# Performance work log

Hardware: AMD Instinct MI355X
Metric: run time of the kernel (lower is better)

The kernel has to match this reference:

```python
import jax, jax.numpy as jnp
import numpy as np

D_MODEL = 1024
N_LAYERS = 4
N_HEADS = 16
HEAD_DIM = 64
FF_DIM = 4096
INNER = N_HEADS * HEAD_DIM  # 1024
SCALE = HEAD_DIM ** -0.5
EPS = 1e-5


def layernorm(x, scale, bias):
    mu = jnp.mean(x, axis=-1, keepdims=True)
    var = jnp.mean(jnp.square(x - mu), axis=-1, keepdims=True)
    return (x - mu) * jax.lax.rsqrt(var + EPS) * scale + bias


def setup_inputs() -> dict:
    key = jax.random.key(0)
    ks = jax.random.split(key, 8)
    b, n = 2, 2048
    s = lambda fan_in: 1.0 / np.sqrt(fan_in)
    inp = {
        "x": jax.random.normal(ks[0], (b, n, D_MODEL), dtype=jnp.float32),
        "Wqkv": jax.random.normal(ks[1], (N_LAYERS, D_MODEL, 3 * INNER), dtype=jnp.float32) * s(D_MODEL),
        "Wout": jax.random.normal(ks[2], (N_LAYERS, INNER, D_MODEL), dtype=jnp.float32) * s(INNER),
        "ln1_s": jnp.ones((N_LAYERS, D_MODEL), jnp.float32),
        "ln1_b": jnp.zeros((N_LAYERS, D_MODEL), jnp.float32),
        "W1": jax.random.normal(ks[3], (N_LAYERS, D_MODEL, FF_DIM), dtype=jnp.float32) * s(D_MODEL),
        "b1": jnp.zeros((N_LAYERS, FF_DIM), jnp.float32),
        "W2": jax.random.normal(ks[4], (N_LAYERS, FF_DIM, D_MODEL), dtype=jnp.float32) * s(FF_DIM),
        "b2": jnp.zeros((N_LAYERS, D_MODEL), jnp.float32),
        "ln2_s": jnp.ones((N_LAYERS, D_MODEL), jnp.float32),
        "ln2_b": jnp.zeros((N_LAYERS, D_MODEL), jnp.float32),
        "lnf_s": jnp.ones((D_MODEL,), jnp.float32),
        "lnf_b": jnp.zeros((D_MODEL,), jnp.float32),
    }
    return inp


def reference(x, Wqkv, Wout, ln1_s, ln1_b, W1, b1, W2, b2, ln2_s, ln2_b, lnf_s, lnf_b):
    b, n, _ = x.shape
    for i in range(N_LAYERS):
        # --- attention block (pre-norm, residual) ---
        h = layernorm(x, ln1_s[i], ln1_b[i])
        qkv = h @ Wqkv[i]                                  # [b, n, 3*inner]
        q, k, v = jnp.split(qkv, 3, axis=-1)
        def heads(t):
            return t.reshape(b, n, N_HEADS, HEAD_DIM).transpose(0, 2, 1, 3)  # b h n d
        q, k, v = heads(q), heads(k), heads(v)
        dots = jnp.einsum('bhnd,bhmd->bhnm', q, k) * SCALE
        attn = jax.nn.softmax(dots, axis=-1)
        out = jnp.einsum('bhnm,bhmd->bhnd', attn, v)
        out = out.transpose(0, 2, 1, 3).reshape(b, n, INNER)
        x = out @ Wout[i] + x
        # --- feedforward block (pre-norm, residual) ---
        h = layernorm(x, ln2_s[i], ln2_b[i])
        h = jax.nn.gelu(h @ W1[i] + b1[i], approximate=False)  # torch GELU default = exact erf
        x = h @ W2[i] + b2[i] + x
    return layernorm(x, lnf_s, lnf_b)
```

## Files before the change

### kernel.cpp

```cpp
#include <hip/hip_runtime.h>
#include <math.h>

#define D_MODEL 1024
#define N_LAYERS 4
#define N_HEADS 16
#define HEAD_DIM 64
#define FF_DIM 4096
#define INNER 1024
#define QKV3 3072
#define EPS 1e-5f
#define ATT_SCALE 0.125f

typedef unsigned short u16;
typedef __attribute__((ext_vector_type(8))) short bf16x8;
typedef __attribute__((ext_vector_type(4))) float f32x4;

typedef const void __attribute__((address_space(1)))* gas1_t;
typedef void __attribute__((address_space(3)))* las3_t;

__device__ __forceinline__ void gl_lds16(const void* g, void* l) {
    __builtin_amdgcn_global_load_lds((gas1_t)g, (las3_t)l, 16, 0, 0);
}
__device__ __forceinline__ void lds_fence() {
    asm volatile("s_waitcnt lgkmcnt(0)" ::: "memory");
    __builtin_amdgcn_sched_barrier(0);
}

__device__ __forceinline__ u16 bf_of(float x) {
    unsigned u = __float_as_uint(x);
    unsigned r = (u + 0x7fffu + ((u >> 16) & 1u)) >> 16;
    return (u16)r;
}
__device__ __forceinline__ float f_of_bf(u16 b) {
    return __uint_as_float(((unsigned)b) << 16);
}
__device__ __forceinline__ void split2(float x, u16& h, u16& l) {
    h = bf_of(x);
    l = bf_of(x - f_of_bf(h));
}

template<bool SPLIT>
__global__ __launch_bounds__(256) void ln_kernel(const float* __restrict__ in,
                                                 const float* __restrict__ sc,
                                                 const float* __restrict__ bs,
                                                 float* outf, u16* outh, u16* outl)
{
    int row = blockIdx.x;
    int t = threadIdx.x;
    const float4* x4 = (const float4*)(in + (size_t)row * D_MODEL);
    float4 v = x4[t];
    float sum = v.x + v.y + v.z + v.w;
    float sq  = v.x*v.x + v.y*v.y + v.z*v.z + v.w*v.w;
#pragma unroll
    for (int o = 32; o > 0; o >>= 1) {
        sum += __shfl_xor(sum, o);
        sq  += __shfl_xor(sq, o);
    }
    __shared__ float s1[4], s2[4];
    int w = t >> 6;
    if ((t & 63) == 0) { s1[w] = sum; s2[w] = sq; }
    __syncthreads();
    sum = s1[0] + s1[1] + s1[2] + s1[3];
    sq  = s2[0] + s2[1] + s2[2] + s2[3];
    float mu  = sum * (1.0f / D_MODEL);
    float var = sq * (1.0f / D_MODEL) - mu * mu;
    float rs  = rsqrtf(var + EPS);
    float4 s = ((const float4*)sc)[t];
    float4 b = ((const float4*)bs)[t];
    float o0 = (v.x - mu) * rs * s.x + b.x;
    float o1 = (v.y - mu) * rs * s.y + b.y;
    float o2 = (v.z - mu) * rs * s.z + b.z;
    float o3 = (v.w - mu) * rs * s.w + b.w;
    if (SPLIT) {
        u16 h0,l0,h1,l1,h2,l2,h3,l3;
        split2(o0,h0,l0); split2(o1,h1,l1); split2(o2,h2,l2); split2(o3,h3,l3);
        size_t idx = (size_t)row * D_MODEL + t * 4;
        *(ushort4*)&outh[idx] = make_ushort4(h0,h1,h2,h3);
        *(ushort4*)&outl[idx] = make_ushort4(l0,l1,l2,l3);
    } else {
        ((float4*)(outf + (size_t)row * D_MODEL))[t] = make_float4(o0,o1,o2,o3);
    }
}

__global__ __launch_bounds__(256) void wsplit_kernel(const float* __restrict__ W,
                                                     u16* __restrict__ Th,
                                                     u16* __restrict__ Tl,
                                                     int K, int N)
{
    __shared__ float t[32][33];
    int tx = threadIdx.x & 31, ty = threadIdx.x >> 5;
    int n0 = blockIdx.x * 32, k0 = blockIdx.y * 32;
#pragma unroll
    for (int i = 0; i < 4; i++) {
        int r = ty + i * 8;
        t[r][tx] = W[(size_t)(k0 + r) * N + n0 + tx];
    }
    __syncthreads();
#pragma unroll
    for (int i = 0; i < 4; i++) {
        int r = ty + i * 8;
        float v = t[tx][r];
        u16 h, l; split2(v, h, l);
        size_t idx = (size_t)(n0 + r) * K + k0 + tx;
        Th[idx] = h; Tl[idx] = l;
    }
}

__global__ __launch_bounds__(256) void vtprep(const u16* __restrict__ qh,
                                              const u16* __restrict__ ql,
                                              u16* __restrict__ vth,
                                              u16* __restrict__ vtl, int n)
{
    int bh = blockIdx.y;
    int b = bh >> 4, h = bh & 15;
    int nb = blockIdx.x * 64 + (threadIdx.x >> 6) * 16;
    int d = threadIdx.x & 63;
    const u16* srcH = qh + (size_t)(b * n + nb) * QKV3 + 2 * INNER + h * HEAD_DIM + d;
    const u16* srcL = ql + (size_t)(b * n + nb) * QKV3 + 2 * INNER + h * HEAD_DIM + d;
    u16 bh_[16], bl_[16];
#pragma unroll
    for (int i = 0; i < 16; i++) {
        bh_[i] = srcH[(size_t)i * QKV3];
        bl_[i] = srcL[(size_t)i * QKV3];
    }
    size_t drow = ((size_t)bh * HEAD_DIM + d) * n + nb;
    *(uint4*)&vth[drow]     = *(uint4*)&bh_[0];
    *(uint4*)&vth[drow + 8] = *(uint4*)&bh_[8];
    *(uint4*)&vtl[drow]     = *(uint4*)&bl_[0];
    *(uint4*)&vtl[drow + 8] = *(uint4*)&bl_[8];
}

#define MFMA_BF16 __builtin_amdgcn_mfma_f32_16x16x32_bf16

template<bool BIAS, bool RES, bool GELU_, bool SPLITOUT>
__global__ __launch_bounds__(256, 2) void mfma_gemm(
    const u16* __restrict__ Ah, const u16* __restrict__ Al,
    const u16* __restrict__ Bh, const u16* __restrict__ Bl,
    const float* __restrict__ bias, const float* res,
    float* Cf, u16* Ch, u16* Cl,
    int M, int N, int K)
{
    __shared__ u16 Asm[128 * 64];
    __shared__ u16 Bsm[128 * 64];
    const int tid = threadIdx.x;
    const int bm0 = blockIdx.y * 128, bn0 = blockIdx.x * 128;
    const int wave = tid >> 6, lane = tid & 63;
    const int wm0 = (wave >> 1) * 64, wn0 = (wave & 1) * 64;
    const int fr = lane & 15, fp = lane >> 4;

    const u16* srcA[4]; const u16* srcB[4];
    u16* dstA[4]; u16* dstB[4];
#pragma unroll
    for (int s = 0; s < 4; s++) {
        int t_ = wave * 4 + s;
        int c  = t_ * 64 + lane;
        int r  = c >> 3;
        int q  = (c & 7) ^ (r & 7);
        const u16* Asel = (q & 4) ? Al : Ah;
        const u16* Bsel = (q & 4) ? Bl : Bh;
        srcA[s] = Asel + (size_t)(bm0 + r) * K + (q & 3) * 8;
        srcB[s] = Bsel + (size_t)(bn0 + r) * K + (q & 3) * 8;
        dstA[s] = &Asm[t_ * 512];
        dstB[s] = &Bsm[t_ * 512];
    }

    const bf16x8 *pAh[4], *pAl[4], *pBh[4], *pBl[4];
#pragma unroll
    for (int i = 0; i < 4; i++) {
        int Ra = wm0 + i * 16 + fr, Rb = wn0 + i * 16 + fr;
        int s7 = fr & 7;
        pAh[i] = (const bf16x8*)&Asm[(Ra * 8 + (fp ^ s7)) * 8];
        pAl[i] = (const bf16x8*)&Asm[(Ra * 8 + ((fp + 4) ^ s7)) * 8];
        pBh[i] = (const bf16x8*)&Bsm[(Rb * 8 + (fp ^ s7)) * 8];
        pBl[i] = (const bf16x8*)&Bsm[(Rb * 8 + ((fp + 4) ^ s7)) * 8];
    }

    f32x4 acc[4][4];
#pragma unroll
    for (int i = 0; i < 4; i++)
#pragma unroll
        for (int j = 0; j < 4; j++)
#pragma unroll
            for (int q = 0; q < 4; q++) acc[i][j][q] = 0.0f;

    for (int k0 = 0; k0 < K; k0 += 32) {
        __syncthreads();
#pragma unroll
        for (int s = 0; s < 4; s++) {
            gl_lds16(srcA[s] + k0, dstA[s]);
            gl_lds16(srcB[s] + k0, dstB[s]);
        }
        __syncthreads();

        bf16x8 fah[4], fal[4], fbh[4], fbl[4];
#pragma unroll
        for (int i = 0; i < 4; i++) {
            fah[i] = *pAh[i]; fal[i] = *pAl[i];
            fbh[i] = *pBh[i]; fbl[i] = *pBl[i];
        }
#pragma unroll
        for (int i = 0; i < 4; i++)
#pragma unroll
            for (int j = 0; j < 4; j++) {
                acc[i][j] = MFMA_BF16(fah[i], fbh[j], acc[i][j], 0, 0, 0);
                acc[i][j] = MFMA_BF16(fah[i], fbl[j], acc[i][j], 0, 0, 0);
                acc[i][j] = MFMA_BF16(fal[i], fbh[j], acc[i][j], 0, 0, 0);
            }
    }

#pragma unroll
    for (int i = 0; i < 4; i++)
#pragma unroll
        for (int j = 0; j < 4; j++) {
            int col = bn0 + wn0 + j * 16 + fr;
            float bv = BIAS ? bias[col] : 0.0f;
#pragma unroll
            for (int q = 0; q < 4; q++) {
                int row = bm0 + wm0 + i * 16 + fp * 4 + q;
                float t = acc[i][j][q] + bv;
                if (GELU_) t = 0.5f * t * (1.0f + erff(t * 0.70710678118654752f));
                if (RES) t += res[(size_t)row * N + col];
                size_t idx = (size_t)row * N + col;
                if (SPLITOUT) { u16 h, l; split2(t, h, l); Ch[idx] = h; Cl[idx] = l; }
                else Cf[idx] = t;
            }
        }
}

__global__ __launch_bounds__(256, 2) void attn_mfma(
    const u16* __restrict__ qh, const u16* __restrict__ ql,
    const u16* __restrict__ vth, const u16* __restrict__ vtl,
    u16* __restrict__ oh, u16* __restrict__ ol, int n, int qblocks)
{
    __shared__ u16 Kt[2][64 * 64];
    __shared__ u16 Vt[2][64 * 64];
    __shared__ u16 Pb[4][2][16 * 64];

    int total = gridDim.x;
    int per_xcd = total >> 3;
    int g = blockIdx.x;
    int flat = (g & 7) * per_xcd + (g >> 3);
    int bh = flat / qblocks;
    int qb = flat - bh * qblocks;
    int b = bh >> 4, h = bh & 15;
    int q0 = qb * 64;

    const int tid = threadIdx.x;
    const int wave = tid >> 6, lane = tid & 63;
    const int q_ = lane & 15, qx = q_ & 7;

    bf16x8 qfh[2], qfl[2];
    {
        size_t qo = (size_t)(b * n + q0 + wave * 16 + q_) * QKV3
                  + h * HEAD_DIM + (lane >> 4) * 8;
        qfh[0] = *(const bf16x8*)&qh[qo];
        qfh[1] = *(const bf16x8*)&qh[qo + 32];
        qfl[0] = *(const bf16x8*)&ql[qo];
        qfl[1] = *(const bf16x8*)&ql[qo + 32];
    }

    f32x4 oa[4];
#pragma unroll
    for (int dt = 0; dt < 4; dt++)
#pragma unroll
        for (int r = 0; r < 4; r++) oa[dt][r] = 0.0f;
    float mreg = -1e30f, lreg = 0.0f;

    for (int j0 = 0; j0 < n; j0 += 64) {
        __syncthreads();
#pragma unroll
        for (int e = 0; e < 8; e++) {
            int ei = wave * 8 + e;
            int half = (ei >> 3) & 1;
            int cb = ei & 7;
            int c = cb * 64 + lane;
            int r = c >> 3;
            int p = (c & 7) ^ (r & 7);
            if (ei < 16) {
                const u16* src = (half ? ql : qh)
                    + (size_t)(b * n + j0 + r) * QKV3 + INNER + h * HEAD_DIM + p * 8;
                gl_lds16(src, &Kt[half][cb * 512]);
            } else {
                const u16* src = (half ? vtl : vth)
                    + ((size_t)bh * HEAD_DIM + r) * n + j0 + p * 8;
                gl_lds16(src, &Vt[half][cb * 512]);
            }
        }
        __syncthreads();

        f32x4 sa[4];
#pragma unroll
        for (int jt = 0; jt < 4; jt++) {
#pragma unroll
            for (int r = 0; r < 4; r++) sa[jt][r] = 0.0f;
            int jr = jt * 16 + q_;
            int ro = jr * 64, x7 = jr & 7;
#pragma unroll
            for (int ks = 0; ks < 2; ks++) {
                int sl = (ks * 4 + (lane >> 4)) ^ x7;
                bf16x8 kh_ = *(const bf16x8*)&Kt[0][ro + sl * 8];
                bf16x8 kl_ = *(const bf16x8*)&Kt[1][ro + sl * 8];
                sa[jt] = MFMA_BF16(kh_, qfh[ks], sa[jt], 0, 0, 0);
                sa[jt] = MFMA_BF16(kh_, qfl[ks], sa[jt], 0, 0, 0);
                sa[jt] = MFMA_BF16(kl_, qfh[ks], sa[jt], 0, 0, 0);
            }
        }

        float p[16];
        float mt = -1e30f;
#pragma unroll
        for (int jt = 0; jt < 4; jt++)
#pragma unroll
            for (int r = 0; r < 4; r++) {
                float sv = sa[jt][r] * ATT_SCALE;
                p[jt * 4 + r] = sv;
                mt = fmaxf(mt, sv);
            }
        mt = fmaxf(mt, __shfl_xor(mt, 16));
        mt = fmaxf(mt, __shfl_xor(mt, 32));
        float mn = fmaxf(mreg, mt);
        float al = __expf(mreg - mn);
        float ps = 0.0f;
#pragma unroll
        for (int t = 0; t < 16; t++) { p[t] = __expf(p[t] - mn); ps += p[t]; }
        ps += __shfl_xor(ps, 16);
        ps += __shfl_xor(ps, 32);
        lreg = lreg * al + ps;
        mreg = mn;
#pragma unroll
        for (int dt = 0; dt < 4; dt++)
#pragma unroll
            for (int r = 0; r < 4; r++) oa[dt][r] *= al;

#pragma unroll
        for (int jt = 0; jt < 4; jt++) {
            int jb = jt * 16 + (lane >> 4) * 4;
            int uo = q_ * 64 + (((jb >> 3) ^ qx) * 8) + (jb & 7);
            ushort4 wh, wl;
            split2(p[jt * 4 + 0], wh.x, wl.x);
            split2(p[jt * 4 + 1], wh.y, wl.y);
            split2(p[jt * 4 + 2], wh.z, wl.z);
            split2(p[jt * 4 + 3], wh.w, wl.w);
            *(ushort4*)&Pb[wave][0][uo] = wh;
            *(ushort4*)&Pb[wave][1][uo] = wl;
        }
        lds_fence();

#pragma unroll
        for (int dt = 0; dt < 4; dt++) {
            int dr = dt * 16 + q_;
            int rv = dr * 64, d7 = dr & 7;
#pragma unroll
            for (int js = 0; js < 2; js++) {
                int sl = js * 4 + (lane >> 4);
                bf16x8 vh_ = *(const bf16x8*)&Vt[0][rv + ((sl ^ d7) * 8)];
                bf16x8 vl_ = *(const bf16x8*)&Vt[1][rv + ((sl ^ d7) * 8)];
                int po = q_ * 64 + ((sl ^ qx) * 8);
                bf16x8 ph_ = *(const bf16x8*)&Pb[wave][0][po];
                bf16x8 pl_ = *(const bf16x8*)&Pb[wave][1][po];
                oa[dt] = MFMA_BF16(vh_, ph_, oa[dt], 0, 0, 0);
                oa[dt] = MFMA_BF16(vh_, pl_, oa[dt], 0, 0, 0);
                oa[dt] = MFMA_BF16(vl_, ph_, oa[dt], 0, 0, 0);
            }
        }
    }

    float inv = 1.0f / lreg;
#pragma unroll
    for (int dt = 0; dt < 4; dt++) {
        int db = dt * 16 + (lane >> 4) * 4;
        int uo = q_ * 64 + (((db >> 3) ^ qx) * 8) + (db & 7);
        ushort4 wh, wl;
        split2(oa[dt][0] * inv, wh.x, wl.x);
        split2(oa[dt][1] * inv, wh.y, wl.y);
        split2(oa[dt][2] * inv, wh.z, wl.z);
        split2(oa[dt][3] * inv, wh.w, wl.w);
        *(ushort4*)&Pb[wave][0][uo] = wh;
        *(ushort4*)&Pb[wave][1][uo] = wl;
    }
    lds_fence();
#pragma unroll
    for (int pass = 0; pass < 2; pass++) {
        int qq = lane >> 2;
        int sl = (lane & 3) + pass * 4;
        int uo = qq * 64 + ((sl ^ (qq & 7)) * 8);
        bf16x8 vh_ = *(const bf16x8*)&Pb[wave][0][uo];
        bf16x8 vl_ = *(const bf16x8*)&Pb[wave][1][uo];
        size_t orow = (size_t)(b * n + q0 + wave * 16 + qq) * INNER
                    + h * HEAD_DIM + sl * 8;
        *(bf16x8*)&oh[orow] = vh_;
        *(bf16x8*)&ol[orow] = vl_;
    }
}

extern "C" void kernel_launch(void* const* d_in, const int* in_sizes, int n_in,
                              void* d_out, int out_size, void* d_ws, size_t ws_size,
                              hipStream_t stream)
{
    const float* x_in   = (const float*)d_in[0];
    const float* Wqkv   = (const float*)d_in[1];
    const float* Wout   = (const float*)d_in[2];
    const float* ln1_s  = (const float*)d_in[3];
    const float* ln1_b  = (const float*)d_in[4];
    const float* W1     = (const float*)d_in[5];
    const float* b1     = (const float*)d_in[6];
    const float* W2     = (const float*)d_in[7];
    const float* b2     = (const float*)d_in[8];
    const float* ln2_s  = (const float*)d_in[9];
    const float* ln2_b  = (const float*)d_in[10];
    const float* lnf_s  = (const float*)d_in[11];
    const float* lnf_b  = (const float*)d_in[12];
    float* outp = (float*)d_out;

    int rows = in_sizes[0] / D_MODEL;
    int n = 2048;
    int batch = rows / n;
    int nbh = batch * N_HEADS;
    int qblocks = n / 64;

    char* p = (char*)d_ws;
    float* x = (float*)p;  p += (size_t)rows * D_MODEL * 4;
    u16* hh  = (u16*)p;    p += (size_t)rows * D_MODEL * 2;
    u16* hl  = (u16*)p;    p += (size_t)rows * D_MODEL * 2;
    u16* qkvh = (u16*)p;
    u16* ffh  = (u16*)p;   p += (size_t)rows * FF_DIM * 2;
    u16* qkvl = (u16*)p;
    u16* ffl  = (u16*)p;   p += (size_t)rows * FF_DIM * 2;
    u16* vth = (u16*)p;    p += (size_t)nbh * HEAD_DIM * n * 2;
    u16* vtl = (u16*)p;    p += (size_t)nbh * HEAD_DIM * n * 2;
    u16* wbh = (u16*)p;    p += (size_t)FF_DIM * D_MODEL * 2;
    u16* wbl = (u16*)p;    p += (size_t)FF_DIM * D_MODEL * 2;

    hipMemcpyAsync(x, x_in, (size_t)rows * D_MODEL * 4, hipMemcpyDeviceToDevice, stream);

    dim3 blk(256);
    for (int i = 0; i < N_LAYERS; i++) {
        const float* Wqkv_i = Wqkv + (size_t)i * D_MODEL * QKV3;
        const float* Wout_i = Wout + (size_t)i * INNER * D_MODEL;
        const float* W1_i   = W1 + (size_t)i * D_MODEL * FF_DIM;
        const float* W2_i   = W2 + (size_t)i * FF_DIM * D_MODEL;

        wsplit_kernel<<<dim3(QKV3/32, D_MODEL/32), blk, 0, stream>>>(Wqkv_i, wbh, wbl, D_MODEL, QKV3);
        ln_kernel<true><<<rows, blk, 0, stream>>>(x, ln1_s + i*D_MODEL, ln1_b + i*D_MODEL,
                                                  nullptr, hh, hl);
        mfma_gemm<false,false,false,true><<<dim3(QKV3/128, rows/128), blk, 0, stream>>>(
            hh, hl, wbh, wbl, nullptr, nullptr, nullptr, qkvh, qkvl, rows, QKV3, D_MODEL);
        vtprep<<<dim3(n/64, nbh), blk, 0, stream>>>(qkvh, qkvl, vth, vtl, n);
        attn_mfma<<<nbh * qblocks, blk, 0, stream>>>(qkvh, qkvl, vth, vtl, hh, hl, n, qblocks);
        wsplit_kernel<<<dim3(D_MODEL/32, INNER/32), blk, 0, stream>>>(Wout_i, wbh, wbl, INNER, D_MODEL);
        mfma_gemm<false,true,false,false><<<dim3(D_MODEL/128, rows/128), blk, 0, stream>>>(
            hh, hl, wbh, wbl, nullptr, x, x, nullptr, nullptr, rows, D_MODEL, INNER);

        ln_kernel<true><<<rows, blk, 0, stream>>>(x, ln2_s + i*D_MODEL, ln2_b + i*D_MODEL,
                                                  nullptr, hh, hl);
        wsplit_kernel<<<dim3(FF_DIM/32, D_MODEL/32), blk, 0, stream>>>(W1_i, wbh, wbl, D_MODEL, FF_DIM);
        mfma_gemm<true,false,true,true><<<dim3(FF_DIM/128, rows/128), blk, 0, stream>>>(
            hh, hl, wbh, wbl, b1 + (size_t)i*FF_DIM, nullptr, nullptr, ffh, ffl,
            rows, FF_DIM, D_MODEL);
        wsplit_kernel<<<dim3(D_MODEL/32, FF_DIM/32), blk, 0, stream>>>(W2_i, wbh, wbl, FF_DIM, D_MODEL);
        mfma_gemm<true,true,false,false><<<dim3(D_MODEL/128, rows/128), blk, 0, stream>>>(
            ffh, ffl, wbh, wbl, b2 + (size_t)i*D_MODEL, x, x, nullptr, nullptr,
            rows, D_MODEL, FF_DIM);
    }
    ln_kernel<false><<<rows, blk, 0, stream>>>(x, lnf_s, lnf_b, outp, nullptr, nullptr);
}
```

Before: 2.669 ms.

## Double-buffer GEMM LDS tiles and remap blocks for XCD-aware grouped tile order

The MFMA GEMM now keeps two LDS buffers so the global-to-LDS loads for the next K slice are issued before computing the current slice, with one barrier per iteration instead of two. The 2D grid becomes a 1D grid whose block index is permuted across the 8 XCDs and then grouped into gm-row super-tiles, so that neighbouring blocks on the same die share A/B tiles in L2. Shared memory doubles to 64KB per block, which may limit occupancy at two blocks per CU. The remap assumes the block count is divisible by 8 and by gm*ntn.

```diff
diff --git a/kernel.cpp b/kernel.cpp
--- a/kernel.cpp
+++ b/kernel.cpp
@@ -138,12 +138,22 @@
     const u16* __restrict__ Bh, const u16* __restrict__ Bl,
     const float* __restrict__ bias, const float* res,
     float* Cf, u16* Ch, u16* Cl,
-    int M, int N, int K)
-{
-    __shared__ u16 Asm[128 * 64];
-    __shared__ u16 Bsm[128 * 64];
+    int M, int N, int K, int gm)
+{
+    __shared__ u16 Asm[2][128 * 64];
+    __shared__ u16 Bsm[2][128 * 64];
+
+    int nwg = gridDim.x;
+    int qq = nwg >> 3;
+    int wg = (blockIdx.x & 7) * qq + (blockIdx.x >> 3);
+    int ntn = N >> 7;
+    int pg = gm * ntn;
+    int grp = wg / pg, rem = wg - grp * pg;
+    int mt = grp * gm + (rem % gm);
+    int nt = rem / gm;
+    const int bm0 = mt << 7, bn0 = nt << 7;
+
     const int tid = threadIdx.x;
-    const int bm0 = blockIdx.y * 128, bn0 = blockIdx.x * 128;
     const int wave = tid >> 6, lane = tid & 63;
     const int wm0 = (wave >> 1) * 64, wn0 = (wave & 1) * 64;
     const int fr = lane & 15, fp = lane >> 4;
@@ -160,19 +170,19 @@
         const u16* Bsel = (q & 4) ? Bl : Bh;
         srcA[s] = Asel + (size_t)(bm0 + r) * K + (q & 3) * 8;
         srcB[s] = Bsel + (size_t)(bn0 + r) * K + (q & 3) * 8;
-        dstA[s] = &Asm[t_ * 512];
-        dstB[s] = &Bsm[t_ * 512];
-    }
-
-    const bf16x8 *pAh[4], *pAl[4], *pBh[4], *pBl[4];
+        dstA[s] = &Asm[0][t_ * 512];
+        dstB[s] = &Bsm[0][t_ * 512];
+    }
+
+    int oAh[4], oAl[4], oBh[4], oBl[4];
 #pragma unroll
     for (int i = 0; i < 4; i++) {
         int Ra = wm0 + i * 16 + fr, Rb = wn0 + i * 16 + fr;
         int s7 = fr & 7;
-        pAh[i] = (const bf16x8*)&Asm[(Ra * 8 + (fp ^ s7)) * 8];
-        pAl[i] = (const bf16x8*)&Asm[(Ra * 8 + ((fp + 4) ^ s7)) * 8];
-        pBh[i] = (const bf16x8*)&Bsm[(Rb * 8 + (fp ^ s7)) * 8];
-        pBl[i] = (const bf16x8*)&Bsm[(Rb * 8 + ((fp + 4) ^ s7)) * 8];
+        oAh[i] = (Ra * 8 + (fp ^ s7)) * 8;
+        oAl[i] = (Ra * 8 + ((fp + 4) ^ s7)) * 8;
+        oBh[i] = (Rb * 8 + (fp ^ s7)) * 8;
+        oBl[i] = (Rb * 8 + ((fp + 4) ^ s7)) * 8;
     }
 
     f32x4 acc[4][4];
@@ -183,30 +193,43 @@
 #pragma unroll
             for (int q = 0; q < 4; q++) acc[i][j][q] = 0.0f;
 
-    for (int k0 = 0; k0 < K; k0 += 32) {
+#define STAGE(B, K0) do { \
+    _Pragma("unroll") \
+    for (int s = 0; s < 4; s++) { \
+        gl_lds16(srcA[s] + (K0), dstA[s] + (B) * 8192); \
+        gl_lds16(srcB[s] + (K0), dstB[s] + (B) * 8192); \
+    } } while (0)
+
+#define COMPUTE(B) do { \
+    bf16x8 fah[4], fal[4], fbh[4], fbl[4]; \
+    _Pragma("unroll") \
+    for (int i = 0; i < 4; i++) { \
+        fah[i] = *(const bf16x8*)&Asm[B][oAh[i]]; \
+        fal[i] = *(const bf16x8*)&Asm[B][oAl[i]]; \
+        fbh[i] = *(const bf16x8*)&Bsm[B][oBh[i]]; \
+        fbl[i] = *(const bf16x8*)&Bsm[B][oBl[i]]; \
+    } \
+    _Pragma("unroll") \
+    for (int i = 0; i < 4; i++) \
+    _Pragma("unroll") \
+        for (int j = 0; j < 4; j++) { \
+            acc[i][j] = MFMA_BF16(fah[i], fbh[j], acc[i][j], 0, 0, 0); \
+            acc[i][j] = MFMA_BF16(fah[i], fbl[j], acc[i][j], 0, 0, 0); \
+            acc[i][j] = MFMA_BF16(fal[i], fbh[j], acc[i][j], 0, 0, 0); \
+        } } while (0)
+
+    STAGE(0, 0);
+    __syncthreads();
+    int cur = 0;
+    for (int k0 = 32; k0 < K; k0 += 32) {
+        STAGE(cur ^ 1, k0);
+        COMPUTE(cur);
         __syncthreads();
-#pragma unroll
-        for (int s = 0; s < 4; s++) {
-            gl_lds16(srcA[s] + k0, dstA[s]);
-            gl_lds16(srcB[s] + k0, dstB[s]);
-        }
-        __syncthreads();
-
-        bf16x8 fah[4], fal[4], fbh[4], fbl[4];
-#pragma unroll
-        for (int i = 0; i < 4; i++) {
-            fah[i] = *pAh[i]; fal[i] = *pAl[i];
-            fbh[i] = *pBh[i]; fbl[i] = *pBl[i];
-        }
-#pragma unroll
-        for (int i = 0; i < 4; i++)
-#pragma unroll
-            for (int j = 0; j < 4; j++) {
-                acc[i][j] = MFMA_BF16(fah[i], fbh[j], acc[i][j], 0, 0, 0);
-                acc[i][j] = MFMA_BF16(fah[i], fbl[j], acc[i][j], 0, 0, 0);
-                acc[i][j] = MFMA_BF16(fal[i], fbh[j], acc[i][j], 0, 0, 0);
-            }
-    }
+        cur ^= 1;
+    }
+    COMPUTE(cur);
+#undef STAGE
+#undef COMPUTE
 
 #pragma unroll
     for (int i = 0; i < 4; i++)
@@ -434,6 +457,7 @@
     hipMemcpyAsync(x, x_in, (size_t)rows * D_MODEL * 4, hipMemcpyDeviceToDevice, stream);
 
     dim3 blk(256);
+    int ntm = rows / 128;
     for (int i = 0; i < N_LAYERS; i++) {
         const float* Wqkv_i = Wqkv + (size_t)i * D_MODEL * QKV3;
         const float* Wout_i = Wout + (size_t)i * INNER * D_MODEL;
@@ -443,24 +467,24 @@
         wsplit_kernel<<<dim3(QKV3/32, D_MODEL/32), blk, 0, stream>>>(Wqkv_i, wbh, wbl, D_MODEL, QKV3);
         ln_kernel<true><<<rows, blk, 0, stream>>>(x, ln1_s + i*D_MODEL, ln1_b + i*D_MODEL,
                                                   nullptr, hh, hl);
-        mfma_gemm<false,false,false,true><<<dim3(QKV3/128, rows/128), blk, 0, stream>>>(
-            hh, hl, wbh, wbl, nullptr, nullptr, nullptr, qkvh, qkvl, rows, QKV3, D_MODEL);
+        mfma_gemm<false,false,false,true><<<ntm * (QKV3/128), blk, 0, stream>>>(
+            hh, hl, wbh, wbl, nullptr, nullptr, nullptr, qkvh, qkvl, rows, QKV3, D_MODEL, 4);
         vtprep<<<dim3(n/64, nbh), blk, 0, stream>>>(qkvh, qkvl, vth, vtl, n);
         attn_mfma<<<nbh * qblocks, blk, 0, stream>>>(qkvh, qkvl, vth, vtl, hh, hl, n, qblocks);
         wsplit_kernel<<<dim3(D_MODEL/32, INNER/32), blk, 0, stream>>>(Wout_i, wbh, wbl, INNER, D_MODEL);
-        mfma_gemm<false,true,false,false><<<dim3(D_MODEL/128, rows/128), blk, 0, stream>>>(
-            hh, hl, wbh, wbl, nullptr, x, x, nullptr, nullptr, rows, D_MODEL, INNER);
+        mfma_gemm<false,true,false,false><<<ntm * (D_MODEL/128), blk, 0, stream>>>(
+            hh, hl, wbh, wbl, nullptr, x, x, nullptr, nullptr, rows, D_MODEL, INNER, 4);
 
         ln_kernel<true><<<rows, blk, 0, stream>>>(x, ln2_s + i*D_MODEL, ln2_b + i*D_MODEL,
                                                   nullptr, hh, hl);
         wsplit_kernel<<<dim3(FF_DIM/32, D_MODEL/32), blk, 0, stream>>>(W1_i, wbh, wbl, D_MODEL, FF_DIM);
-        mfma_gemm<true,false,true,true><<<dim3(FF_DIM/128, rows/128), blk, 0, stream>>>(
+        mfma_gemm<true,false,true,true><<<ntm * (FF_DIM/128), blk, 0, stream>>>(
             hh, hl, wbh, wbl, b1 + (size_t)i*FF_DIM, nullptr, nullptr, ffh, ffl,
-            rows, FF_DIM, D_MODEL);
+            rows, FF_DIM, D_MODEL, 4);
         wsplit_kernel<<<dim3(D_MODEL/32, FF_DIM/32), blk, 0, stream>>>(W2_i, wbh, wbl, FF_DIM, D_MODEL);
-        mfma_gemm<true,true,false,false><<<dim3(D_MODEL/128, rows/128), blk, 0, stream>>>(
+        mfma_gemm<true,true,false,false><<<ntm * (D_MODEL/128), blk, 0, stream>>>(
             ffh, ffl, wbh, wbl, b2 + (size_t)i*D_MODEL, x, x, nullptr, nullptr,
-            rows, D_MODEL, FF_DIM);
+            rows, D_MODEL, FF_DIM, 2);
     }
     ln_kernel<false><<<rows, blk, 0, stream>>>(x, lnf_s, lnf_b, outp, nullptr, nullptr);
 }
```

Result: no change. 2.654 ms (-0.6%).
